# Kernel tuning notes

Measured on AMD Instinct MI355X. Metric: run time of the kernel, lower is better.

The kernel has to match this reference:

```python
import jax, jax.numpy as jnp
import numpy as np

D_MODEL = 1024
N_HEADS = 16
D_K = D_MODEL // N_HEADS
B, L = 2, 2048


def setup_inputs() -> dict:
    key = jax.random.key(0)
    ks = jax.random.split(key, 13)
    s = 0.02
    inp = {
        'query': jax.random.normal(ks[0], (B, L, D_MODEL), jnp.float32),
        'key': jax.random.normal(ks[1], (B, L, D_MODEL), jnp.float32),
        'value': jax.random.normal(ks[2], (B, L, D_MODEL), jnp.float32),
        'mask': jax.random.randint(ks[3], (1, 1, L, L), 0, 2).astype(bool),
        'W_q': jax.random.normal(ks[4], (D_MODEL, D_MODEL), jnp.float32) * s,
        'b_q': jnp.zeros((D_MODEL,), jnp.float32),
        'W_k': jax.random.normal(ks[5], (D_MODEL, D_MODEL), jnp.float32) * s,
        'b_k': jnp.zeros((D_MODEL,), jnp.float32),
        'W_v': jax.random.normal(ks[6], (D_MODEL, D_MODEL), jnp.float32) * s,
        'b_v': jnp.zeros((D_MODEL,), jnp.float32),
        'W_o': jax.random.normal(ks[7], (D_MODEL, D_MODEL), jnp.float32) * s,
        'b_o': jnp.zeros((D_MODEL,), jnp.float32),
    }
    return inp


def _split_heads(x):
    b, l, _ = x.shape
    return x.reshape(b, l, N_HEADS, D_K).transpose(0, 2, 1, 3)  # [B,H,L,dk]


def reference(query, key, value, mask, W_q, b_q, W_k, b_k, W_v, b_v, W_o, b_o):
    q = _split_heads(query @ W_q + b_q)
    k = _split_heads(key @ W_k + b_k)
    v = _split_heads(value @ W_v + b_v)
    # Unscaled attention logits [B,H,L,L] (NO 1/sqrt(dk))
    logits = jnp.einsum('bhqd,bhkd->bhqk', q, k)
    logits = jnp.where(mask, -jnp.inf, logits)
    w = jax.nn.softmax(logits, axis=-1)
    w = jnp.nan_to_num(w, nan=0.0)  # fully-masked rows -> zeros
    attended = jnp.einsum('bhqk,bhkd->bhqd', w, v)
    # dropout in eval mode = identity; combine heads
    out = attended.transpose(0, 2, 1, 3).reshape(B, L, D_MODEL)
    return out @ W_o + b_o
```

## Files before the change

### kernel.cpp

```cpp
#include <hip/hip_runtime.h>
#include <hip/hip_bf16.h>
#include <stdint.h>


typedef __bf16 bf16;
typedef __bf16 bf16x8 __attribute__((ext_vector_type(8)));
typedef float f32x4 __attribute__((ext_vector_type(4)));

#define AS1 __attribute__((address_space(1)))
#define AS3 __attribute__((address_space(3)))

__device__ __forceinline__ void g2l16(const void* g, void* l) {
    __builtin_amdgcn_global_load_lds((AS1 void*)g, (AS3 void*)l, 16, 0, 0);
}

__device__ __forceinline__ bool lane_masked(unsigned long long m) {
#if __has_builtin(__builtin_amdgcn_inverse_ballot_w64)
    return __builtin_amdgcn_inverse_ballot_w64(m);
#else
    return (m >> (threadIdx.x & 63)) & 1ull;
#endif
}

#define LOG2E 1.44269504088896f

__global__ __launch_bounds__(256) void prep_kernel(
    const float* __restrict__ q, const float* __restrict__ k, const float* __restrict__ v,
    bf16* xq, bf16* xk, bf16* xv,
    const float* W0, const float* W1, const float* W2, const float* W3,
    bf16* T0, bf16* T1, bf16* T2, bf16* T3,
    const unsigned int* __restrict__ mask, unsigned long long* __restrict__ rmb) {
    __shared__ __align__(16) bf16 t[64 * 72];
    int y = blockIdx.y;
    int tid = threadIdx.x;
    if (y < 3) {
        const float* in = (y == 0) ? q : (y == 1) ? k : v;
        bf16* out = (y == 0) ? xq : (y == 1) ? xk : xv;
        int idx = blockIdx.x * 256 + tid;
        float4 vv = ((const float4*)in)[idx];
        __align__(8) bf16 o[4];
        o[0] = (bf16)vv.x; o[1] = (bf16)vv.y; o[2] = (bf16)vv.z; o[3] = (bf16)vv.w;
        *(uint2*)(out + (size_t)idx * 4) = *(const uint2*)o;
        return;
    }
    int bx = blockIdx.x;
    if (bx >= 2048) return;
    if (bx >= 1024) {
        int task = (bx - 1024) * 4 + (tid >> 6);
        int qg = task >> 5, kt = task & 31;
        int lane = tid & 63, quad = lane >> 4, col = lane & 15;
        int row0 = qg * 16 + quad * 4;
        int c0 = kt * 64 + col;
        #pragma unroll
        for (int r = 0; r < 4; ++r) {
            const unsigned int* mrow = mask + (size_t)(row0 + r) * 2048;
            #pragma unroll
            for (int nt = 0; nt < 4; ++nt) {
                unsigned long long b = __ballot(mrow[c0 + nt * 16] != 0u);
                if (lane == 0) rmb[(size_t)task * 16 + r * 4 + nt] = b;
            }
        }
        return;
    }
    const float* W; bf16* T;
    int wi = bx >> 8;
    if (wi == 0)      { W = W0; T = T0; }
    else if (wi == 1) { W = W1; T = T1; }
    else if (wi == 2) { W = W2; T = T2; }
    else              { W = W3; T = T3; }
    int x = bx & 255;
    int tx = x & 15, ty = x >> 4;
    int n0 = tx * 64, k0 = ty * 64;
    #pragma unroll
    for (int rr = 0; rr < 4; ++rr) {
        int idx = rr * 256 + tid;
        int r = idx >> 4, c4 = (idx & 15) * 4;
        float4 vv = *(const float4*)(W + (size_t)(k0 + r) * 1024 + n0 + c4);
        __align__(8) bf16 o[4];
        o[0] = (bf16)vv.x; o[1] = (bf16)vv.y; o[2] = (bf16)vv.z; o[3] = (bf16)vv.w;
        *(uint2*)&t[r * 72 + c4] = *(const uint2*)o;
    }
    __syncthreads();
    #pragma unroll
    for (int rr = 0; rr < 2; ++rr) {
        int idx = rr * 256 + tid;
        int n = idx >> 3, kc = (idx & 7) * 8;
        __align__(16) bf16 o[8];
        #pragma unroll
        for (int j = 0; j < 8; ++j) o[j] = t[(kc + j) * 72 + n];
        *(uint4*)(T + (size_t)(n0 + n) * 1024 + k0 + kc) = *(const uint4*)o;
    }
}

template <int MODE>
__device__ __forceinline__ void gemm128_core(const bf16* __restrict__ A,
                                             const bf16* __restrict__ Bt,
                                             const float* __restrict__ bias,
                                             void* __restrict__ Out, int bm, int bn,
                                             float scale) {
    __shared__ __align__(16) bf16 la[128 * 64];
    __shared__ __align__(16) bf16 lb[128 * 64];
    int tid = threadIdx.x;
    int w = tid >> 6, lane = tid & 63;
    int quad = lane >> 4, col = lane & 15;
    int c7 = col & 7;
    int wm = w >> 1, wn = w & 1;
    int m0 = bm * 128, n0 = bn * 128;
    f32x4 acc[4][4];
    f32x4 z = {0.f, 0.f, 0.f, 0.f};
    #pragma unroll
    for (int i = 0; i < 4; ++i)
        #pragma unroll
        for (int j = 0; j < 4; ++j) acc[i][j] = z;
    int sr = lane >> 3;
    int sg = (lane & 7) ^ sr;
    int swz0 = (quad ^ c7) * 8;
    int swz1 = ((4 + quad) ^ c7) * 8;
    for (int kt = 0; kt < 16; ++kt) {
        int kk = kt * 64;
        __syncthreads();
        #pragma unroll
        for (int i = 0; i < 4; ++i) {
            int ch = w * 4 + i;
            int row = ch * 8 + sr;
            g2l16(A + (size_t)(m0 + row) * 1024 + kk + sg * 8, &la[ch * 512]);
            g2l16(Bt + (size_t)(n0 + row) * 1024 + kk + sg * 8, &lb[ch * 512]);
        }
        __syncthreads();
        bf16x8 af[4][2], bfr[4][2];
        #pragma unroll
        for (int mt = 0; mt < 4; ++mt) {
            af[mt][0] = *(const bf16x8*)&la[(wm * 64 + mt * 16 + col) * 64 + swz0];
            af[mt][1] = *(const bf16x8*)&la[(wm * 64 + mt * 16 + col) * 64 + swz1];
        }
        #pragma unroll
        for (int nt = 0; nt < 4; ++nt) {
            bfr[nt][0] = *(const bf16x8*)&lb[(wn * 64 + nt * 16 + col) * 64 + swz0];
            bfr[nt][1] = *(const bf16x8*)&lb[(wn * 64 + nt * 16 + col) * 64 + swz1];
        }
        #pragma unroll
        for (int mt = 0; mt < 4; ++mt)
            #pragma unroll
            for (int nt = 0; nt < 4; ++nt) {
                acc[mt][nt] = __builtin_amdgcn_mfma_f32_16x16x32_bf16(
                    af[mt][0], bfr[nt][0], acc[mt][nt], 0, 0, 0);
                acc[mt][nt] = __builtin_amdgcn_mfma_f32_16x16x32_bf16(
                    af[mt][1], bfr[nt][1], acc[mt][nt], 0, 0, 0);
            }
    }
    float bia[4];
    #pragma unroll
    for (int nt = 0; nt < 4; ++nt) bia[nt] = bias[n0 + wn * 64 + nt * 16 + col];
    #pragma unroll
    for (int mt = 0; mt < 4; ++mt) {
        #pragma unroll
        for (int nt = 0; nt < 4; ++nt) {
            #pragma unroll
            for (int r = 0; r < 4; ++r) {
                int m = m0 + wm * 64 + mt * 16 + quad * 4 + r;
                int n = n0 + wn * 64 + nt * 16 + col;
                float v = (acc[mt][nt][r] + bia[nt]) * scale;
                if (MODE == 0) {
                    int b = m >> 11, l = m & 2047, h = n >> 6, d = n & 63;
                    ((bf16*)Out)[(((size_t)b * 16 + h) * 2048 + l) * 64 + d] = (bf16)v;
                } else {
                    int b = m >> 11, l = m & 2047, h = n >> 6, d = n & 63;
                    ((bf16*)Out)[(((size_t)b * 16 + h) * 64 + d) * 2048 + l] = (bf16)v;
                }
            }
        }
    }
}

__global__ __launch_bounds__(256) void qkv_kernel(
    const bf16* Xq, const bf16* Xk, const bf16* Xv,
    const bf16* Wq, const bf16* Wk, const bf16* Wv,
    const float* bq, const float* bk, const float* bv,
    bf16* Qh, bf16* Kh, bf16* Vt) {
    int y = blockIdx.y;
    int bm = blockIdx.x >> 3, bn = blockIdx.x & 7;
    if (y == 0)      gemm128_core<0>(Xq, Wq, bq, Qh, bm, bn, LOG2E);
    else if (y == 1) gemm128_core<0>(Xk, Wk, bk, Kh, bm, bn, 1.0f);
    else             gemm128_core<2>(Xv, Wv, bv, Vt, bm, bn, 1.0f);
}

__global__ __launch_bounds__(256) void ogemm_kernel(const bf16* __restrict__ A,
                                                    const bf16* __restrict__ Wt,
                                                    const float* __restrict__ bias,
                                                    float* __restrict__ Out) {
    int bm = blockIdx.x >> 3, bn = blockIdx.x & 7;
    __shared__ __align__(16) bf16 la[64 * 64];
    __shared__ __align__(16) bf16 lb[128 * 64];
    int tid = threadIdx.x;
    int w = tid >> 6, lane = tid & 63;
    int quad = lane >> 4, col = lane & 15;
    int c7 = col & 7;
    int m0 = bm * 64, n0 = bn * 128;
    f32x4 acc[4][2];
    f32x4 z = {0.f, 0.f, 0.f, 0.f};
    #pragma unroll
    for (int i = 0; i < 4; ++i) { acc[i][0] = z; acc[i][1] = z; }
    int sr = lane >> 3;
    int sg = (lane & 7) ^ sr;
    int swz0 = (quad ^ c7) * 8;
    int swz1 = ((4 + quad) ^ c7) * 8;
    for (int kt = 0; kt < 16; ++kt) {
        int kk = kt * 64;
        __syncthreads();
        #pragma unroll
        for (int i = 0; i < 2; ++i) {
            int ch = w * 2 + i;
            g2l16(A + (size_t)(m0 + ch * 8 + sr) * 1024 + kk + sg * 8, &la[ch * 512]);
        }
        #pragma unroll
        for (int i = 0; i < 4; ++i) {
            int ch = w * 4 + i;
            g2l16(Wt + (size_t)(n0 + ch * 8 + sr) * 1024 + kk + sg * 8, &lb[ch * 512]);
        }
        __syncthreads();
        bf16x8 af[4][2], bfr[2][2];
        #pragma unroll
        for (int mt = 0; mt < 4; ++mt) {
            af[mt][0] = *(const bf16x8*)&la[(mt * 16 + col) * 64 + swz0];
            af[mt][1] = *(const bf16x8*)&la[(mt * 16 + col) * 64 + swz1];
        }
        #pragma unroll
        for (int nt = 0; nt < 2; ++nt) {
            bfr[nt][0] = *(const bf16x8*)&lb[(w * 32 + nt * 16 + col) * 64 + swz0];
            bfr[nt][1] = *(const bf16x8*)&lb[(w * 32 + nt * 16 + col) * 64 + swz1];
        }
        #pragma unroll
        for (int mt = 0; mt < 4; ++mt)
            #pragma unroll
            for (int nt = 0; nt < 2; ++nt) {
                acc[mt][nt] = __builtin_amdgcn_mfma_f32_16x16x32_bf16(
                    af[mt][0], bfr[nt][0], acc[mt][nt], 0, 0, 0);
                acc[mt][nt] = __builtin_amdgcn_mfma_f32_16x16x32_bf16(
                    af[mt][1], bfr[nt][1], acc[mt][nt], 0, 0, 0);
            }
    }
    float bia[2];
    bia[0] = bias[n0 + w * 32 + col];
    bia[1] = bias[n0 + w * 32 + 16 + col];
    #pragma unroll
    for (int mt = 0; mt < 4; ++mt)
        #pragma unroll
        for (int nt = 0; nt < 2; ++nt)
            #pragma unroll
            for (int r = 0; r < 4; ++r)
                Out[(size_t)(m0 + mt * 16 + quad * 4 + r) * 1024 +
                    n0 + w * 32 + nt * 16 + col] = acc[mt][nt][r] + bia[nt];
}

__global__ __launch_bounds__(128) void attn_kernel(const bf16* __restrict__ Qh,
                                                   const bf16* __restrict__ Kh,
                                                   const bf16* __restrict__ Vt,
                                                   const unsigned long long* __restrict__ rmb,
                                                   bf16* __restrict__ att) {
    int bh = blockIdx.x, qt = blockIdx.y;
    int b = bh >> 4, h = bh & 15;
    int q0 = qt * 64;
    __shared__ __align__(16) bf16 ks[64 * 64];
    __shared__ __align__(16) bf16 vs[64 * 64];
    __shared__ __align__(16) bf16 ps[2 * 32 * 72];
    int tid = threadIdx.x;
    int w = tid >> 6, lane = tid & 63;
    int quad = lane >> 4, col = lane & 15;
    int c7 = col & 7;
    int sr = lane >> 3;
    int sg = (lane & 7) ^ sr;
    int swz0 = (quad ^ c7) * 8;
    int swz1 = ((4 + quad) ^ c7) * 8;

    int mofs = __builtin_amdgcn_readfirstlane((qt * 4 + w * 2) * 512);

    #pragma unroll
    for (int i = 0; i < 4; ++i) {
        int ch = w * 4 + i;
        g2l16(Qh + ((size_t)bh * 2048 + q0 + ch * 8 + sr) * 64 + sg * 8, &ks[ch * 512]);
    }
    __syncthreads();
    bf16x8 aq[2][2];
    #pragma unroll
    for (int mt = 0; mt < 2; ++mt) {
        aq[mt][0] = *(const bf16x8*)&ks[(w * 32 + mt * 16 + col) * 64 + swz0];
        aq[mt][1] = *(const bf16x8*)&ks[(w * 32 + mt * 16 + col) * 64 + swz1];
    }
    bf16x8 onesf;
    #pragma unroll
    for (int i = 0; i < 8; ++i) onesf[i] = (bf16)1.0f;

    f32x4 z = {0.f, 0.f, 0.f, 0.f};
    f32x4 O[2][4], R[2];
    #pragma unroll
    for (int mt = 0; mt < 2; ++mt) {
        R[mt] = z;
        #pragma unroll
        for (int i = 0; i < 4; ++i) O[mt][i] = z;
    }

    for (int kt = 0; kt < 32; ++kt) {
        __syncthreads();
        #pragma unroll
        for (int i = 0; i < 4; ++i) {
            int ch = w * 4 + i;
            int r = ch * 8 + sr;
            g2l16(Kh + ((size_t)bh * 2048 + kt * 64 + r) * 64 + sg * 8, &ks[ch * 512]);
            g2l16(Vt + ((size_t)bh * 64 + r) * 2048 + kt * 64 + sg * 8, &vs[ch * 512]);
        }
        __syncthreads();

        f32x4 s[2][4];
        #pragma unroll
        for (int nt = 0; nt < 4; ++nt) {
            s[0][nt] = z; s[1][nt] = z;
            bf16x8 bk0 = *(const bf16x8*)&ks[(nt * 16 + col) * 64 + swz0];
            s[0][nt] = __builtin_amdgcn_mfma_f32_16x16x32_bf16(aq[0][0], bk0, s[0][nt], 0, 0, 0);
            s[1][nt] = __builtin_amdgcn_mfma_f32_16x16x32_bf16(aq[1][0], bk0, s[1][nt], 0, 0, 0);
            bf16x8 bk1 = *(const bf16x8*)&ks[(nt * 16 + col) * 64 + swz1];
            s[0][nt] = __builtin_amdgcn_mfma_f32_16x16x32_bf16(aq[0][1], bk1, s[0][nt], 0, 0, 0);
            s[1][nt] = __builtin_amdgcn_mfma_f32_16x16x32_bf16(aq[1][1], bk1, s[1][nt], 0, 0, 0);
        }

        #pragma unroll
        for (int mt = 0; mt < 2; ++mt) {
            const unsigned long long* mw = rmb + mofs + mt * 512 + kt * 16;
            #pragma unroll
            for (int r = 0; r < 4; ++r) {
                #pragma unroll
                for (int nt = 0; nt < 4; ++nt) {
                    float p = __builtin_amdgcn_exp2f(s[mt][nt][r]);
                    if (lane_masked(mw[r * 4 + nt])) p = 0.0f;
                    ps[w * 2304 + (mt * 16 + quad * 4 + r) * 72 + nt * 16 + col] = (bf16)p;
                }
            }
        }

        bf16x8 ap[2][2];
        #pragma unroll
        for (int mt = 0; mt < 2; ++mt) {
            ap[mt][0] = *(const bf16x8*)&ps[w * 2304 + (mt * 16 + col) * 72 + quad * 8];
            ap[mt][1] = *(const bf16x8*)&ps[w * 2304 + (mt * 16 + col) * 72 + 32 + quad * 8];
        }
        #pragma unroll
        for (int dt = 0; dt < 4; ++dt) {
            bf16x8 bv0 = *(const bf16x8*)&vs[(dt * 16 + col) * 64 + swz0];
            O[0][dt] = __builtin_amdgcn_mfma_f32_16x16x32_bf16(ap[0][0], bv0, O[0][dt], 0, 0, 0);
            O[1][dt] = __builtin_amdgcn_mfma_f32_16x16x32_bf16(ap[1][0], bv0, O[1][dt], 0, 0, 0);
            bf16x8 bv1 = *(const bf16x8*)&vs[(dt * 16 + col) * 64 + swz1];
            O[0][dt] = __builtin_amdgcn_mfma_f32_16x16x32_bf16(ap[0][1], bv1, O[0][dt], 0, 0, 0);
            O[1][dt] = __builtin_amdgcn_mfma_f32_16x16x32_bf16(ap[1][1], bv1, O[1][dt], 0, 0, 0);
        }
        #pragma unroll
        for (int mt = 0; mt < 2; ++mt) {
            R[mt] = __builtin_amdgcn_mfma_f32_16x16x32_bf16(ap[mt][0], onesf, R[mt], 0, 0, 0);
            R[mt] = __builtin_amdgcn_mfma_f32_16x16x32_bf16(ap[mt][1], onesf, R[mt], 0, 0, 0);
        }
    }

    #pragma unroll
    for (int mt = 0; mt < 2; ++mt) {
        #pragma unroll
        for (int r = 0; r < 4; ++r) {
            float rsv = R[mt][r];
            float inv = (rsv > 0.f) ? 1.0f / rsv : 0.f;
            int qg = q0 + w * 32 + mt * 16 + quad * 4 + r;
            #pragma unroll
            for (int dt = 0; dt < 4; ++dt) {
                float ov = O[mt][dt][r] * inv;
                att[((size_t)b * 2048 + qg) * 1024 + h * 64 + dt * 16 + col] = (bf16)ov;
            }
        }
    }
}

extern "C" void kernel_launch(void* const* d_in, const int* in_sizes, int n_in,
                              void* d_out, int out_size, void* d_ws, size_t ws_size,
                              hipStream_t stream) {
    (void)in_sizes; (void)n_in; (void)out_size; (void)ws_size;
    const float* query = (const float*)d_in[0];
    const float* key_  = (const float*)d_in[1];
    const float* value = (const float*)d_in[2];
    const void*  mask  = d_in[3];
    const float* W_q = (const float*)d_in[4];
    const float* b_q = (const float*)d_in[5];
    const float* W_k = (const float*)d_in[6];
    const float* b_k = (const float*)d_in[7];
    const float* W_v = (const float*)d_in[8];
    const float* b_v = (const float*)d_in[9];
    const float* W_o = (const float*)d_in[10];
    const float* b_o = (const float*)d_in[11];

    char* ws = (char*)d_ws;
    bf16* Xq  = (bf16*)(ws + 0);
    bf16* Xk  = (bf16*)(ws + 8388608);
    bf16* Xv  = (bf16*)(ws + 16777216);
    bf16* Wtq = (bf16*)(ws + 25165824);
    bf16* Wtk = (bf16*)(ws + 27262976);
    bf16* Wtv = (bf16*)(ws + 29360128);
    bf16* Wto = (bf16*)(ws + 31457280);
    bf16* Qh  = (bf16*)(ws + 33554432);
    bf16* Kh  = (bf16*)(ws + 41943040);
    bf16* Vt  = (bf16*)(ws + 50331648);
    bf16* att = (bf16*)(ws + 58720256);
    unsigned long long* rmb = (unsigned long long*)(ws + 67633152);

    prep_kernel<<<dim3(4096, 4), 256, 0, stream>>>(query, key_, value, Xq, Xk, Xv,
                                                   W_q, W_k, W_v, W_o,
                                                   Wtq, Wtk, Wtv, Wto,
                                                   (const unsigned int*)mask, rmb);

    qkv_kernel<<<dim3(256, 3), 256, 0, stream>>>(Xq, Xk, Xv, Wtq, Wtk, Wtv,
                                                 b_q, b_k, b_v, Qh, Kh, Vt);
    attn_kernel<<<dim3(32, 32), 128, 0, stream>>>(Qh, Kh, Vt, rmb, att);
    ogemm_kernel<<<512, 256, 0, stream>>>(att, Wto, b_o, (float*)d_out);
}
```

Before: 267.1 us.

## Split attention over key range with fp32 partials and a reduction kernel

```diff
diff --git a/kernel.cpp b/kernel.cpp
--- a/kernel.cpp
+++ b/kernel.cpp
@@ -252,12 +252,17 @@
                     n0 + w * 32 + nt * 16 + col] = acc[mt][nt][r] + bia[nt];
 }
 
-__global__ __launch_bounds__(128) void attn_kernel(const bf16* __restrict__ Qh,
-                                                   const bf16* __restrict__ Kh,
-                                                   const bf16* __restrict__ Vt,
-                                                   const unsigned long long* __restrict__ rmb,
-                                                   bf16* __restrict__ att) {
+template <int SPLIT>
+__device__ __forceinline__ void attn_core(const bf16* __restrict__ Qh,
+                                          const bf16* __restrict__ Kh,
+                                          const bf16* __restrict__ Vt,
+                                          const unsigned long long* __restrict__ rmb,
+                                          bf16* __restrict__ att,
+                                          float* __restrict__ Opart,
+                                          float* __restrict__ Rpart) {
     int bh = blockIdx.x, qt = blockIdx.y;
+    int half = SPLIT ? blockIdx.z : 0;
+    int kt0 = half * 16, nkt = SPLIT ? 16 : 32;
     int b = bh >> 4, h = bh & 15;
     int q0 = qt * 64;
     __shared__ __align__(16) bf16 ks[64 * 64];
@@ -299,7 +304,8 @@
         for (int i = 0; i < 4; ++i) O[mt][i] = z;
     }
 
-    for (int kt = 0; kt < 32; ++kt) {
+    for (int it = 0; it < nkt; ++it) {
+        int kt = kt0 + it;
         __syncthreads();
         #pragma unroll
         for (int i = 0; i < 4; ++i) {
@@ -362,22 +368,68 @@
     for (int mt = 0; mt < 2; ++mt) {
         #pragma unroll
         for (int r = 0; r < 4; ++r) {
-            float rsv = R[mt][r];
-            float inv = (rsv > 0.f) ? 1.0f / rsv : 0.f;
-            int qg = q0 + w * 32 + mt * 16 + quad * 4 + r;
-            #pragma unroll
-            for (int dt = 0; dt < 4; ++dt) {
-                float ov = O[mt][dt][r] * inv;
-                att[((size_t)b * 2048 + qg) * 1024 + h * 64 + dt * 16 + col] = (bf16)ov;
-            }
-        }
-    }
+            int row = w * 32 + mt * 16 + quad * 4 + r;
+            int qg = q0 + row;
+            if (SPLIT) {
+                if (col == 0) Rpart[((size_t)half * 32 + bh) * 2048 + qg] = R[mt][r];
+                #pragma unroll
+                for (int dt = 0; dt < 4; ++dt)
+                    Opart[(((size_t)(half * 2 + b) * 2048 + qg) * 1024) +
+                          h * 64 + dt * 16 + col] = O[mt][dt][r];
+            } else {
+                float rsv = R[mt][r];
+                float inv = (rsv > 0.f) ? 1.0f / rsv : 0.f;
+                #pragma unroll
+                for (int dt = 0; dt < 4; ++dt) {
+                    float ov = O[mt][dt][r] * inv;
+                    att[((size_t)b * 2048 + qg) * 1024 + h * 64 + dt * 16 + col] = (bf16)ov;
+                }
+            }
+        }
+    }
+}
+
+__global__ __launch_bounds__(128) void attn_kernel(const bf16* __restrict__ Qh,
+                                                   const bf16* __restrict__ Kh,
+                                                   const bf16* __restrict__ Vt,
+                                                   const unsigned long long* __restrict__ rmb,
+                                                   bf16* __restrict__ att) {
+    attn_core<0>(Qh, Kh, Vt, rmb, att, nullptr, nullptr);
+}
+
+__global__ __launch_bounds__(128) void attn_split_kernel(const bf16* __restrict__ Qh,
+                                                         const bf16* __restrict__ Kh,
+                                                         const bf16* __restrict__ Vt,
+                                                         const unsigned long long* __restrict__ rmb,
+                                                         float* __restrict__ Opart,
+                                                         float* __restrict__ Rpart) {
+    attn_core<1>(Qh, Kh, Vt, rmb, nullptr, Opart, Rpart);
+}
+
+__global__ __launch_bounds__(256) void reduce_kernel(const float* __restrict__ Opart,
+                                                     const float* __restrict__ Rpart,
+                                                     bf16* __restrict__ att) {
+    size_t flat = ((size_t)blockIdx.x * 256 + threadIdx.x) * 4;
+    float4 o0 = *(const float4*)(Opart + flat);
+    float4 o1 = *(const float4*)(Opart + 4194304 + flat);
+    int bl = (int)(flat >> 10);
+    int h = ((int)flat & 1023) >> 6;
+    int b = bl >> 11, l = bl & 2047;
+    int bh = b * 16 + h;
+    float r = Rpart[(size_t)bh * 2048 + l] + Rpart[65536 + (size_t)bh * 2048 + l];
+    float inv = (r > 0.f) ? 1.0f / r : 0.f;
+    __align__(8) bf16 o[4];
+    o[0] = (bf16)(o0.x + o1.x) * (bf16)1.0f, o[0] = (bf16)((o0.x + o1.x) * inv);
+    o[1] = (bf16)((o0.y + o1.y) * inv);
+    o[2] = (bf16)((o0.z + o1.z) * inv);
+    o[3] = (bf16)((o0.w + o1.w) * inv);
+    *(uint2*)(att + flat) = *(const uint2*)o;
 }
 
 extern "C" void kernel_launch(void* const* d_in, const int* in_sizes, int n_in,
                               void* d_out, int out_size, void* d_ws, size_t ws_size,
                               hipStream_t stream) {
-    (void)in_sizes; (void)n_in; (void)out_size; (void)ws_size;
+    (void)in_sizes; (void)n_in; (void)out_size;
     const float* query = (const float*)d_in[0];
     const float* key_  = (const float*)d_in[1];
     const float* value = (const float*)d_in[2];
@@ -404,6 +456,9 @@
     bf16* Vt  = (bf16*)(ws + 50331648);
     bf16* att = (bf16*)(ws + 58720256);
     unsigned long long* rmb = (unsigned long long*)(ws + 67633152);
+    float* Opart = (float*)(ws + 68157440);
+    float* Rpart = (float*)(ws + 68157440 + 33554432);
+    const size_t WS_NEEDED = 68157440ull + 33554432ull + 524288ull;
 
     prep_kernel<<<dim3(4096, 4), 256, 0, stream>>>(query, key_, value, Xq, Xk, Xv,
                                                    W_q, W_k, W_v, W_o,
@@ -412,6 +467,12 @@
 
     qkv_kernel<<<dim3(256, 3), 256, 0, stream>>>(Xq, Xk, Xv, Wtq, Wtk, Wtv,
                                                  b_q, b_k, b_v, Qh, Kh, Vt);
-    attn_kernel<<<dim3(32, 32), 128, 0, stream>>>(Qh, Kh, Vt, rmb, att);
+    if (ws_size >= WS_NEEDED) {
+        attn_split_kernel<<<dim3(32, 32, 2), 128, 0, stream>>>(Qh, Kh, Vt, rmb,
+                                                               Opart, Rpart);
+        reduce_kernel<<<4096, 256, 0, stream>>>(Opart, Rpart, att);
+    } else {
+        attn_kernel<<<dim3(32, 32), 128, 0, stream>>>(Qh, Kh, Vt, rmb, att);
+    }
     ogemm_kernel<<<512, 256, 0, stream>>>(att, Wto, b_o, (float*)d_out);
 }
```

Result: slower. 301.3 us (+12.8%).
